# Kernel tuning notes

Hardware: AMD Instinct MI355X
Metric: run time of the kernel (lower is better)

Reference implementation:

```python
import jax, jax.numpy as jnp
import numpy as np

N_NODES = 20000
N_EDGES = 100000
STALK_DIM = 32
N_EDGE_ATTR = 32
N_FEAT = 32


def setup_inputs() -> dict:
    key = jax.random.key(0)
    k1, k2, k3, k4 = jax.random.split(key, 4)
    x = jax.random.normal(k1, (N_NODES, STALK_DIM, N_FEAT), dtype=jnp.float32)
    edge_index = jax.random.randint(k2, (2, N_EDGES), 0, N_NODES, dtype=jnp.int64)
    edge_attr = jax.random.normal(k3, (N_EDGES, N_EDGE_ATTR), dtype=jnp.float32)
    # basis restriction maps: (n_edge_attr, 2, d, d), scaled by 1/stalk_dim as in __init__
    restriction_maps = jax.random.normal(k4, (N_EDGE_ATTR, 2, STALK_DIM, STALK_DIM), dtype=jnp.float32) / STALK_DIM
    return {"x": x, "edge_index": edge_index, "edge_attr": edge_attr, "restriction_maps": restriction_maps}


def reference(x, edge_index, edge_attr, restriction_maps):
    n_nodes, d, _ = x.shape
    n_attr = restriction_maps.shape[0]
    # per-edge restriction maps via linear combination of basis maps
    # F: (E, 2, d, d)
    F = (edge_attr @ restriction_maps.reshape(n_attr, 2 * d * d)).reshape(-1, 2, d, d)
    F_left = F[:, 0]   # (E, d, d)
    F_right = F[:, 1]  # (E, d, d)
    # gather node features onto edges
    x_left = x[edge_index[0]]   # (E, d, f)
    x_right = x[edge_index[1]]  # (E, d, f)
    # coboundary: dx = F_left @ x_left - F_right @ x_right
    dx = jnp.einsum('eij,ejf->eif', F_left, x_left) - jnp.einsum('eij,ejf->eif', F_right, x_right)
    # boundary (delta^T dx): transpose-apply and scatter-add to nodes
    x_e_left = jnp.einsum('eji,ejf->eif', F_left, dx)    # F_left^T @ dx
    x_e_right = jnp.einsum('eji,ejf->eif', F_right, dx)  # F_right^T @ dx
    x_out = jax.ops.segment_sum(x_e_left, edge_index[0], num_segments=n_nodes)
    x_out = x_out - jax.ops.segment_sum(x_e_right, edge_index[1], num_segments=n_nodes)
    return x_out
```

## Files before the change

kernel.cpp:

```cpp
#include <hip/hip_runtime.h>
#include <hip/hip_bf16.h>

#define NN 20000
#define NE 100000
#define NINC (2 * NE)
#define NB (NINC / 16)
#define PGRID 512
#define SLOTS 16
#define FSTRIDE 2056

typedef __attribute__((ext_vector_type(8))) short bf16x8;
typedef __attribute__((ext_vector_type(4))) float f32x4;
typedef __attribute__((ext_vector_type(16))) float f32x16;
typedef __attribute__((ext_vector_type(2))) unsigned uint2v;
typedef __attribute__((ext_vector_type(4))) unsigned uint4v;

#define WS_RBFT 0u
#define WS_FLAG 131072u
#define WS_OFF  131328u
#define WS_CUR  (WS_OFF + 4u*(NN+1))
#define WS_CNT  (WS_CUR + 4u*NN)
#define WS_INC  (WS_CNT + 4u*NN)
#define WS_NODE (WS_INC + 4u*NINC)
#define WS_CSR_END ((size_t)WS_NODE + 4u*NINC)
#define WS_XT   ((WS_CSR_END + 4095u) & ~(size_t)4095u)
#define WS_XT_END (WS_XT + (size_t)NN * 2048u * 2u)
#define WS_PB   ((WS_XT_END + 4095u) & ~(size_t)4095u)
#define WS_PB_END (WS_PB + (size_t)NB * 2u * 2048u)

__device__ __forceinline__ unsigned short f2bf(float f) {
    unsigned u = __float_as_uint(f);
    u += 0x7fffu + ((u >> 16) & 1u);
    return (unsigned short)(u >> 16);
}

__device__ __forceinline__ unsigned pack2bf(float a, float b) {
    union { __hip_bfloat162 h; unsigned u; } q;
    q.h = __float22bfloat162_rn(make_float2(a, b));
    return q.u;
}

__device__ __forceinline__ float bf2f(unsigned s) {
    return __uint_as_float(s << 16);
}

__device__ __forceinline__ bf16x8 bneg8(bf16x8 v) {
    union { bf16x8 s; uint4v u; } a; a.s = v;
    a.u[0] ^= 0x80008000u; a.u[1] ^= 0x80008000u;
    a.u[2] ^= 0x80008000u; a.u[3] ^= 0x80008000u;
    return a.s;
}

__global__ void prep_rbf_kernel(const float* __restrict__ R, unsigned short* __restrict__ RbfT,
                                int* __restrict__ flag) {
    int idx = blockIdx.x * blockDim.x + threadIdx.x;
    if (idx == 0) *flag = 0;
    if (idx >= 2048 * 32) return;
    int pos = idx >> 5;
    int a = idx & 31;
    RbfT[idx] = f2bf(R[a * 2048 + pos]);
}

__global__ void detect_kernel(const unsigned* __restrict__ w, int* __restrict__ flag) {
    int k = blockIdx.x * blockDim.x + threadIdx.x;
    if (k < NE && w[2 * k + 1] != 0) atomicOr(flag, 1);
}

__device__ __forceinline__ void decode_edge(const void* eidx, int use64, int e, int& src, int& dst) {
    if (use64) {
        const long long* p = (const long long*)eidx;
        src = (int)p[e]; dst = (int)p[NE + e];
    } else {
        const int* p = (const int*)eidx;
        src = p[e]; dst = p[NE + e];
    }
}

__global__ void count_kernel(const void* __restrict__ eidx, const int* __restrict__ flag,
                             unsigned* __restrict__ cnt) {
    int e = blockIdx.x * blockDim.x + threadIdx.x;
    if (e >= NE) return;
    int src, dst;
    decode_edge(eidx, *flag == 0, e, src, dst);
    if ((unsigned)src < NN) atomicAdd(&cnt[src], 1u);
    if ((unsigned)dst < NN) atomicAdd(&cnt[dst], 1u);
}

__global__ __launch_bounds__(1024) void scan_kernel(const unsigned* __restrict__ cnt,
                                                    unsigned* __restrict__ off,
                                                    unsigned* __restrict__ cur) {
    __shared__ unsigned sd[1024];
    const int t = threadIdx.x;
    unsigned vals[20];
    unsigned s = 0;
#pragma unroll
    for (int j = 0; j < 20; ++j) {
        int idx = t * 20 + j;
        unsigned v = (idx < NN) ? cnt[idx] : 0u;
        vals[j] = s; s += v;
    }
    sd[t] = s;
    __syncthreads();
    for (int d = 1; d < 1024; d <<= 1) {
        unsigned v = (t >= d) ? sd[t - d] : 0u;
        __syncthreads();
        sd[t] += v;
        __syncthreads();
    }
    unsigned base = (t > 0) ? sd[t - 1] : 0u;
#pragma unroll
    for (int j = 0; j < 20; ++j) {
        int idx = t * 20 + j;
        if (idx < NN) { unsigned o = base + vals[j]; off[idx] = o; cur[idx] = o; }
    }
    if (t == 1023) off[NN] = sd[1023];
}

__global__ void scatter_kernel(const void* __restrict__ eidx, const int* __restrict__ flag,
                               unsigned* __restrict__ cur, unsigned* __restrict__ inc,
                               unsigned* __restrict__ nodeOf) {
    int e = blockIdx.x * blockDim.x + threadIdx.x;
    if (e >= NE) return;
    int src, dst;
    decode_edge(eidx, *flag == 0, e, src, dst);
    if ((unsigned)src < NN) { unsigned p = atomicAdd(&cur[src], 1u); inc[p] = (unsigned)e; nodeOf[p] = (unsigned)src; }
    if ((unsigned)dst < NN) { unsigned p = atomicAdd(&cur[dst], 1u); inc[p] = (unsigned)e | 0x80000000u; nodeOf[p] = (unsigned)dst; }
}

__global__ __launch_bounds__(256) void xpose_kernel(const float* __restrict__ x,
                                                    unsigned short* __restrict__ xT) {
    __shared__ float tile[4][32][33];
    const int t = threadIdx.x, sub = t >> 6, lane = t & 63;
    const int n = blockIdx.x * 4 + sub;
    const int row = lane >> 1, half = (lane & 1) * 16;
    const float* xp = x + (size_t)n * 1024 + row * 32 + half;
    float* tp = &tile[sub][row][half];
#pragma unroll
    for (int c = 0; c < 4; ++c)
        *(f32x4*)(tp + 4 * c) = *(const f32x4*)(xp + 4 * c);
    __syncthreads();
    const int f = lane >> 1, k0 = (lane & 1) * 16;
    unsigned w[8];
#pragma unroll
    for (int m = 0; m < 8; ++m) {
        unsigned lo = (unsigned)f2bf(tile[sub][k0 + 2 * m][f]);
        unsigned hi = (unsigned)f2bf(tile[sub][k0 + 2 * m + 1][f]);
        w[m] = lo | (hi << 16);
    }
    unsigned short* op = xT + (size_t)n * 2048 + f * 32 + k0;
    uint4v v0 = {w[0], w[1], w[2], w[3]};
    uint4v v1 = {w[4], w[5], w[6], w[7]};
    *(uint4v*)op = v0;
    *(uint4v*)(op + 8) = v1;
}

__global__ __launch_bounds__(256, 2) void sheaf_inc(
    const unsigned short* __restrict__ xTbuf,
    const void* __restrict__ eidx_raw,
    const float* __restrict__ ea,
    const unsigned short* __restrict__ RbfT,
    const int* __restrict__ flag,
    const unsigned* __restrict__ off,
    const unsigned* __restrict__ inc,
    const unsigned* __restrict__ nodeOf,
    float* __restrict__ out,
    unsigned short* __restrict__ pbuf)
{
    __shared__ __align__(16) unsigned short F_lds[SLOTS * FSTRIDE];
    __shared__ __align__(16) unsigned dx_lds32[4 * 512];
    __shared__ int slot_src[SLOTS], slot_dst[SLOTS], slot_side[SLOTS], slot_e[SLOTS], slot_n[SLOTS];

    const int tid  = threadIdx.x;
    const int lane = tid & 63;
    const int wv   = tid >> 6;
    const int use64 = (*flag == 0);

    const int r31 = lane & 31;
    const int hi  = lane >> 5;
    const int kb  = hi * 8;
    const int l15 = lane & 15;
    const int ab  = (lane >> 4) * 8;
    const int pg  = (lane >> 4) * 4;
    unsigned* dx2 = dx_lds32 + wv * 512;

    bf16x8 rbft[32];
#pragma unroll
    for (int t = 0; t < 32; ++t)
        rbft[t] = *(const bf16x8*)(RbfT + (size_t)(wv * 512 + t * 16 + l15) * 32 + ab);

    for (int b = blockIdx.x; b < NB; b += PGRID) {
        const int p0 = b * 16;
        __syncthreads();

        if (tid < SLOTS) {
            unsigned v = inc[p0 + tid];
            int e = (int)(v & 0x7fffffffu);
            int s, d; decode_edge(eidx_raw, use64, e, s, d);
            if ((unsigned)s >= NN) s = 0;
            if ((unsigned)d >= NN) d = 0;
            slot_e[tid] = e; slot_src[tid] = s; slot_dst[tid] = d;
            slot_side[tid] = (int)(v >> 31);
            slot_n[tid] = (int)nodeOf[p0 + tid];
        }
        __syncthreads();

        bf16x8 pre0[4], pre1[4], pre2[4], pre3[4];
#pragma unroll
        for (int s = 0; s < 4; ++s) {
            const int si = wv + 4 * s;
            const unsigned short* xls = xTbuf + (size_t)slot_src[si] * 2048 + r31 * 32 + kb;
            const unsigned short* xrs = xTbuf + (size_t)slot_dst[si] * 2048 + r31 * 32 + kb;
            pre0[s] = *(const bf16x8*)xls;
            pre1[s] = *(const bf16x8*)(xls + 16);
            pre2[s] = *(const bf16x8*)xrs;
            pre3[s] = *(const bf16x8*)(xrs + 16);
        }

        {
            const int e = slot_e[l15];
            bf16x8 bfrag;
            {
                const float* eap = ea + (size_t)e * 32 + ab;
                f32x4 a0 = *(const f32x4*)eap;
                f32x4 a1 = *(const f32x4*)(eap + 4);
#pragma unroll
                for (int j = 0; j < 4; ++j) { bfrag[j] = (short)f2bf(a0[j]); bfrag[4 + j] = (short)f2bf(a1[j]); }
            }
            unsigned short* fdst = F_lds + l15 * FSTRIDE;
#pragma unroll
            for (int t = 0; t < 32; ++t) {
                f32x4 c = {0.f, 0.f, 0.f, 0.f};
                c = __builtin_amdgcn_mfma_f32_16x16x32_bf16(rbft[t], bfrag, c, 0, 0, 0);
                const int posb = wv * 512 + t * 16 + pg;
                const int side = posb >> 10;
                const int ijb  = posb & 1023;
                const int i    = ijb >> 5;
                const int soff = ijb ^ ((i & 7) << 3);
                uint2v wp = {pack2bf(c[0], c[1]), pack2bf(c[2], c[3])};
                *(uint2v*)(fdst + side * 1024 + soff) = wp;
            }
        }
        __syncthreads();

#pragma unroll
        for (int s = 0; s < 4; ++s) {
            const int si = wv + 4 * s;
            const int side = slot_side[si];

            bf16x8 xlf0 = pre0[s];
            bf16x8 xlf1 = pre1[s];
            bf16x8 xrf0 = bneg8(pre2[s]);
            bf16x8 xrf1 = bneg8(pre3[s]);

            const unsigned short* Fl = F_lds + si * FSTRIDE;
            const unsigned short* Fr = Fl + 1024;
            const int rbase = r31 * 32;
            const int rsw   = (r31 & 7) << 3;
            bf16x8 fl0 = *(const bf16x8*)(Fl + ((rbase + kb) ^ rsw));
            bf16x8 fl1 = *(const bf16x8*)(Fl + ((rbase + 16 + kb) ^ rsw));
            bf16x8 fr0 = *(const bf16x8*)(Fr + ((rbase + kb) ^ rsw));
            bf16x8 fr1 = *(const bf16x8*)(Fr + ((rbase + 16 + kb) ^ rsw));

            f32x16 dacc;
#pragma unroll
            for (int r = 0; r < 16; ++r) dacc[r] = 0.f;
            dacc = __builtin_amdgcn_mfma_f32_32x32x16_bf16(fl0, xlf0, dacc, 0, 0, 0);
            dacc = __builtin_amdgcn_mfma_f32_32x32x16_bf16(fl1, xlf1, dacc, 0, 0, 0);
            dacc = __builtin_amdgcn_mfma_f32_32x32x16_bf16(fr0, xrf0, dacc, 0, 0, 0);
            dacc = __builtin_amdgcn_mfma_f32_32x32x16_bf16(fr1, xrf1, dacc, 0, 0, 0);

            const unsigned smask = side ? 0x80008000u : 0u;
#pragma unroll
            for (int m = 0; m < 8; ++m) {
                const int wi = (m & 1) + 4 * (m >> 1) + 2 * hi;
                dx2[wi * 32 + r31] = pack2bf(dacc[2 * m], dacc[2 * m + 1]) ^ smask;
            }
            unsigned wa[4], wb[4];
#pragma unroll
            for (int m = 0; m < 4; ++m) {
                wa[m] = dx2[(4 * hi + m) * 32 + r31];
                wb[m] = dx2[(8 + 4 * hi + m) * 32 + r31];
            }
            union { uint4v u; bf16x8 s; } pa, pb;
            pa.u = (uint4v){wa[0], wa[1], wa[2], wa[3]};
            pb.u = (uint4v){wb[0], wb[1], wb[2], wb[3]};
            const bf16x8 dxf0 = pa.s, dxf1 = pb.s;

            const unsigned short* Fs = side ? Fr : Fl;
            bf16x8 fT0, fT1;
#pragma unroll
            for (int j = 0; j < 8; ++j) {
                const int k0 = kb + j, k1 = 16 + kb + j;
                fT0[j] = (short)Fs[(k0 * 32 + r31) ^ ((k0 & 7) << 3)];
                fT1[j] = (short)Fs[(k1 * 32 + r31) ^ ((k1 & 7) << 3)];
            }
            f32x16 y;
#pragma unroll
            for (int r = 0; r < 16; ++r) y[r] = 0.f;
            y = __builtin_amdgcn_mfma_f32_32x32x16_bf16(fT0, dxf0, y, 0, 0, 0);
            y = __builtin_amdgcn_mfma_f32_32x32x16_bf16(fT1, dxf1, y, 0, 0, 0);

            float* ybuf = (float*)(F_lds + si * FSTRIDE);
#pragma unroll
            for (int r = 0; r < 16; ++r) {
                const int row = (r & 3) + 8 * (r >> 2) + 4 * hi;
                ybuf[row * 32 + r31] = y[r];
            }
        }
        __syncthreads();

        {
            const int e4 = tid * 4;
            int segA = 0;
            while (segA < SLOTS) {
                const int n = slot_n[segA];
                int segB = segA + 1;
                while (segB < SLOTS && slot_n[segB] == n) ++segB;
                f32x4 sum = {0.f, 0.f, 0.f, 0.f};
                for (int s2 = segA; s2 < segB; ++s2) {
                    const f32x4 v = *(const f32x4*)((const float*)(F_lds + s2 * FSTRIDE) + e4);
#pragma unroll
                    for (int j = 0; j < 4; ++j) sum[j] += v[j];
                }
                const unsigned on = off[n], on1 = off[n + 1];
                const bool complete = ((unsigned)(p0 + segA) == on) && ((unsigned)(p0 + segB) == on1);
                if (complete) {
                    *(f32x4*)(out + (size_t)n * 1024 + e4) = sum;
                } else {
                    const int idx = (segA == 0) ? 0 : 1;
                    unsigned short* pb = pbuf + ((size_t)b * 2 + idx) * 1024;
                    uint2v wp = {pack2bf(sum[0], sum[1]), pack2bf(sum[2], sum[3])};
                    *(uint2v*)(pb + e4) = wp;
                }
                segA = segB;
            }
        }
    }
}

__global__ __launch_bounds__(256) void combine_kernel(
    const unsigned* __restrict__ off, const unsigned* __restrict__ nodeOf,
    const unsigned short* __restrict__ pbuf, float* __restrict__ out)
{
    const int n = blockIdx.x;
    const int e4 = threadIdx.x * 4;
    const unsigned a = off[n], b = off[n + 1];
    if (a == b) {
        f32x4 z = {0.f, 0.f, 0.f, 0.f};
        *(f32x4*)(out + (size_t)n * 1024 + e4) = z;
        return;
    }
    const unsigned b0 = a >> 4, b1 = (b - 1) >> 4;
    if (b0 == b1) return;
    f32x4 sum = {0.f, 0.f, 0.f, 0.f};
    for (unsigned blk = b0; blk <= b1; ++blk) {
        const int idx = (nodeOf[blk * 16] == (unsigned)n) ? 0 : 1;
        const unsigned short* pb = pbuf + ((size_t)blk * 2 + idx) * 1024;
        uint2v w = *(const uint2v*)(pb + e4);
        sum[0] += bf2f(w[0] & 0xffffu); sum[1] += bf2f(w[0] >> 16);
        sum[2] += bf2f(w[1] & 0xffffu); sum[3] += bf2f(w[1] >> 16);
    }
    *(f32x4*)(out + (size_t)n * 1024 + e4) = sum;
}

template<bool XT>
__global__ __launch_bounds__(256, 2) void sheaf_node(
    const float* __restrict__ x,
    const unsigned short* __restrict__ xTbuf,
    const void* __restrict__ eidx_raw,
    const float* __restrict__ ea,
    const unsigned short* __restrict__ RbfT,
    const int* __restrict__ flag,
    const unsigned* __restrict__ off,
    const unsigned* __restrict__ inc,
    float* __restrict__ out)
{
    __shared__ __align__(16) unsigned short F_lds[SLOTS * FSTRIDE];
    __shared__ __align__(16) unsigned dx_lds32[4 * 512];
    __shared__ int slot_src[SLOTS], slot_dst[SLOTS], slot_side[SLOTS], slot_e[SLOTS];

    const int n    = blockIdx.x;
    const int tid  = threadIdx.x;
    const int lane = tid & 63;
    const int wv   = tid >> 6;
    const int use64 = (*flag == 0);

    const unsigned start = off[n];
    const int deg = (int)(off[n + 1] - start);

    const int r31 = lane & 31;
    const int hi  = lane >> 5;
    const int kb  = hi * 8;
    unsigned* dx2 = dx_lds32 + wv * 512;

    f32x16 acc;
#pragma unroll
    for (int r = 0; r < 16; ++r) acc[r] = 0.f;

    for (int base = 0; base < deg; base += SLOTS) {
        __syncthreads();
        if (tid < SLOTS) {
            int p = base + tid;
            if (p < deg) {
                unsigned v = inc[start + p];
                int e = (int)(v & 0x7fffffffu);
                int s, d; decode_edge(eidx_raw, use64, e, s, d);
                if ((unsigned)s >= NN) s = 0;
                if ((unsigned)d >= NN) d = 0;
                slot_e[tid] = e; slot_src[tid] = s; slot_dst[tid] = d;
                slot_side[tid] = (int)(v >> 31);
            } else slot_e[tid] = -1;
        }
        __syncthreads();

        bf16x8 pre0[4], pre1[4], pre2[4], pre3[4];
        if constexpr (XT) {
#pragma unroll
            for (int s = 0; s < 4; ++s) {
                const int si = wv + 4 * s;
                if (base + si < deg) {
                    const unsigned short* xls = xTbuf + (size_t)slot_src[si] * 2048 + r31 * 32 + kb;
                    const unsigned short* xrs = xTbuf + (size_t)slot_dst[si] * 2048 + r31 * 32 + kb;
                    pre0[s] = *(const bf16x8*)xls;
                    pre1[s] = *(const bf16x8*)(xls + 16);
                    pre2[s] = *(const bf16x8*)xrs;
                    pre3[s] = *(const bf16x8*)(xrs + 16);
                }
            }
        }

        {
            const int slot = lane & 15;
            const int ab   = (lane >> 4) * 8;
            const int e    = slot_e[slot];
            bf16x8 bfrag = {0, 0, 0, 0, 0, 0, 0, 0};
            if (e >= 0) {
                const float* eap = ea + (size_t)e * 32 + ab;
                f32x4 a0 = *(const f32x4*)eap;
                f32x4 a1 = *(const f32x4*)(eap + 4);
#pragma unroll
                for (int j = 0; j < 4; ++j) { bfrag[j] = (short)f2bf(a0[j]); bfrag[4 + j] = (short)f2bf(a1[j]); }
            }
            unsigned short* fdst = F_lds + slot * FSTRIDE;
            const int pg = (lane >> 4) * 4;
#pragma unroll 8
            for (int t = 0; t < 32; ++t) {
                const int pos_base = wv * 512 + t * 16;
                bf16x8 afrag = *(const bf16x8*)(RbfT + (size_t)(pos_base + (lane & 15)) * 32 + ab);
                f32x4 c = {0.f, 0.f, 0.f, 0.f};
                c = __builtin_amdgcn_mfma_f32_16x16x32_bf16(afrag, bfrag, c, 0, 0, 0);
                const int posb = pos_base + pg;
                const int side = posb >> 10;
                const int ijb  = posb & 1023;
                const int i    = ijb >> 5;
                const int soff = ijb ^ ((i & 7) << 3);
                uint2v wp = {pack2bf(c[0], c[1]), pack2bf(c[2], c[3])};
                *(uint2v*)(fdst + side * 1024 + soff) = wp;
            }
        }
        __syncthreads();

#pragma unroll
        for (int s = 0; s < 4; ++s) {
            const int si = wv + 4 * s;
            if (base + si >= deg) break;
            const int src  = slot_src[si];
            const int dst  = slot_dst[si];
            const int side = slot_side[si];

            bf16x8 xlf0, xlf1, xrf0, xrf1;
            if constexpr (XT) {
                xlf0 = pre0[s];
                xlf1 = pre1[s];
                xrf0 = bneg8(pre2[s]);
                xrf1 = bneg8(pre3[s]);
            } else {
                const float* xl = x + (size_t)src * 1024 + r31;
                const float* xr = x + (size_t)dst * 1024 + r31;
#pragma unroll
                for (int j = 0; j < 8; ++j) {
                    xlf0[j] = (short)f2bf(xl[(kb + j) * 32]);
                    xlf1[j] = (short)f2bf(xl[(16 + kb + j) * 32]);
                    xrf0[j] = (short)f2bf(-xr[(kb + j) * 32]);
                    xrf1[j] = (short)f2bf(-xr[(16 + kb + j) * 32]);
                }
            }

            const unsigned short* Fl = F_lds + si * FSTRIDE;
            const unsigned short* Fr = Fl + 1024;
            const int rbase = r31 * 32;
            const int rsw   = (r31 & 7) << 3;
            bf16x8 fl0 = *(const bf16x8*)(Fl + ((rbase + kb) ^ rsw));
            bf16x8 fl1 = *(const bf16x8*)(Fl + ((rbase + 16 + kb) ^ rsw));
            bf16x8 fr0 = *(const bf16x8*)(Fr + ((rbase + kb) ^ rsw));
            bf16x8 fr1 = *(const bf16x8*)(Fr + ((rbase + 16 + kb) ^ rsw));

            f32x16 dacc;
#pragma unroll
            for (int r = 0; r < 16; ++r) dacc[r] = 0.f;
            dacc = __builtin_amdgcn_mfma_f32_32x32x16_bf16(fl0, xlf0, dacc, 0, 0, 0);
            dacc = __builtin_amdgcn_mfma_f32_32x32x16_bf16(fl1, xlf1, dacc, 0, 0, 0);
            dacc = __builtin_amdgcn_mfma_f32_32x32x16_bf16(fr0, xrf0, dacc, 0, 0, 0);
            dacc = __builtin_amdgcn_mfma_f32_32x32x16_bf16(fr1, xrf1, dacc, 0, 0, 0);

            const unsigned smask = side ? 0x80008000u : 0u;
#pragma unroll
            for (int m = 0; m < 8; ++m) {
                const int wi = (m & 1) + 4 * (m >> 1) + 2 * hi;
                dx2[wi * 32 + r31] = pack2bf(dacc[2 * m], dacc[2 * m + 1]) ^ smask;
            }
            unsigned wa[4], wb[4];
#pragma unroll
            for (int m = 0; m < 4; ++m) {
                wa[m] = dx2[(4 * hi + m) * 32 + r31];
                wb[m] = dx2[(8 + 4 * hi + m) * 32 + r31];
            }
            union { uint4v u; bf16x8 s; } pa, pb;
            pa.u = (uint4v){wa[0], wa[1], wa[2], wa[3]};
            pb.u = (uint4v){wb[0], wb[1], wb[2], wb[3]};
            const bf16x8 dxf0 = pa.s, dxf1 = pb.s;

            const unsigned short* Fs = side ? Fr : Fl;
            bf16x8 fT0, fT1;
#pragma unroll
            for (int j = 0; j < 8; ++j) {
                const int k0 = kb + j, k1 = 16 + kb + j;
                fT0[j] = (short)Fs[(k0 * 32 + r31) ^ ((k0 & 7) << 3)];
                fT1[j] = (short)Fs[(k1 * 32 + r31) ^ ((k1 & 7) << 3)];
            }
            acc = __builtin_amdgcn_mfma_f32_32x32x16_bf16(fT0, dxf0, acc, 0, 0, 0);
            acc = __builtin_amdgcn_mfma_f32_32x32x16_bf16(fT1, dxf1, acc, 0, 0, 0);
        }
    }

    __syncthreads();
    float* red = (float*)F_lds;
#pragma unroll
    for (int r = 0; r < 16; ++r) {
        const int row = (r & 3) + 8 * (r >> 2) + 4 * hi;
        red[wv * 1024 + row * 32 + r31] = acc[r];
    }
    __syncthreads();
    {
        const int p4 = tid * 4;
        f32x4 s0 = *(const f32x4*)(red + p4);
        f32x4 s1 = *(const f32x4*)(red + 1024 + p4);
        f32x4 s2 = *(const f32x4*)(red + 2048 + p4);
        f32x4 s3 = *(const f32x4*)(red + 3072 + p4);
        f32x4 o;
#pragma unroll
        for (int j = 0; j < 4; ++j) o[j] = (s0[j] + s1[j]) + (s2[j] + s3[j]);
        *(f32x4*)(out + (size_t)n * 1024 + p4) = o;
    }
}

__global__ __launch_bounds__(512, 4) void sheaf_atomic(
    const float* __restrict__ x,
    const void* __restrict__ eidx_raw,
    const float* __restrict__ ea,
    const unsigned short* __restrict__ RbfT,
    const int* __restrict__ flag,
    float* __restrict__ out)
{
    __shared__ __align__(16) unsigned short F_lds[16 * 2048];
    __shared__ __align__(16) unsigned short dx_lds[8 * 1024];

    const int tid  = threadIdx.x;
    const int lane = tid & 63;
    const int wv   = tid >> 6;
    const int e0   = blockIdx.x * 16;
    const int use64 = (*flag == 0);

    {
        const int arow = lane & 15;
        const int ab   = (lane >> 4) * 8;
        const float* eap = ea + (size_t)(e0 + arow) * 32 + ab;
        f32x4 a0 = *(const f32x4*)eap;
        f32x4 a1 = *(const f32x4*)(eap + 4);
        bf16x8 afrag;
#pragma unroll
        for (int j = 0; j < 4; ++j) { afrag[j] = (short)f2bf(a0[j]); afrag[4 + j] = (short)f2bf(a1[j]); }
        const int pcol  = lane & 15;
        const int ebase = (lane >> 4) * 4;
#pragma unroll
        for (int t = 0; t < 16; ++t) {
            const int pos = wv * 256 + t * 16 + pcol;
            bf16x8 bfrag = *(const bf16x8*)(RbfT + pos * 32 + ab);
            f32x4 c = {0.f, 0.f, 0.f, 0.f};
            c = __builtin_amdgcn_mfma_f32_16x16x32_bf16(afrag, bfrag, c, 0, 0, 0);
            const int side = pos >> 10;
            const int ij   = pos & 1023;
            const int i    = ij >> 5;
            const int soff = side * 1024 + (ij ^ ((i & 7) << 3));
#pragma unroll
            for (int r = 0; r < 4; ++r)
                F_lds[(ebase + r) * 2048 + soff] = f2bf(c[r]);
        }
    }
    __syncthreads();

    const int r31 = lane & 31;
    const int hi  = lane >> 5;
    const int kb  = hi * 8;
    unsigned short* dxb = dx_lds + wv * 1024;

#pragma unroll 1
    for (int sub = 0; sub < 2; ++sub) {
        const int el = wv * 2 + sub;
        const int e  = e0 + el;
        int src, dst;
        decode_edge(eidx_raw, use64, e, src, dst);
        if ((unsigned)src >= NN || (unsigned)dst >= NN) continue;

        const float* xl = x + (size_t)src * 1024 + r31;
        const float* xr = x + (size_t)dst * 1024 + r31;
        bf16x8 xlf0, xlf1, xrf0, xrf1;
#pragma unroll
        for (int j = 0; j < 8; ++j) {
            xlf0[j] = (short)f2bf(xl[(kb + j) * 32]);
            xlf1[j] = (short)f2bf(xl[(16 + kb + j) * 32]);
            xrf0[j] = (short)f2bf(-xr[(kb + j) * 32]);
            xrf1[j] = (short)f2bf(-xr[(16 + kb + j) * 32]);
        }
        const unsigned short* Fl = F_lds + el * 2048;
        const unsigned short* Fr = Fl + 1024;
        const int rbase = r31 * 32;
        const int rsw   = (r31 & 7) << 3;
        bf16x8 fl0 = *(const bf16x8*)(Fl + ((rbase + kb) ^ rsw));
        bf16x8 fl1 = *(const bf16x8*)(Fl + ((rbase + 16 + kb) ^ rsw));
        bf16x8 fr0 = *(const bf16x8*)(Fr + ((rbase + kb) ^ rsw));
        bf16x8 fr1 = *(const bf16x8*)(Fr + ((rbase + 16 + kb) ^ rsw));

        f32x16 dacc;
#pragma unroll
        for (int r = 0; r < 16; ++r) dacc[r] = 0.f;
        dacc = __builtin_amdgcn_mfma_f32_32x32x16_bf16(fl0, xlf0, dacc, 0, 0, 0);
        dacc = __builtin_amdgcn_mfma_f32_32x32x16_bf16(fl1, xlf1, dacc, 0, 0, 0);
        dacc = __builtin_amdgcn_mfma_f32_32x32x16_bf16(fr0, xrf0, dacc, 0, 0, 0);
        dacc = __builtin_amdgcn_mfma_f32_32x32x16_bf16(fr1, xrf1, dacc, 0, 0, 0);

#pragma unroll
        for (int r = 0; r < 16; ++r) {
            const int row = (r & 3) + 8 * (r >> 2) + 4 * hi;
            dxb[row * 32 + r31] = f2bf(dacc[r]);
        }
        bf16x8 dxf0, dxf1;
#pragma unroll
        for (int j = 0; j < 8; ++j) {
            dxf0[j] = (short)dxb[(kb + j) * 32 + r31];
            dxf1[j] = (short)dxb[(16 + kb + j) * 32 + r31];
        }

        bf16x8 flT0, flT1;
#pragma unroll
        for (int j = 0; j < 8; ++j) {
            const int k0 = kb + j, k1 = 16 + kb + j;
            flT0[j] = (short)Fl[(k0 * 32 + r31) ^ ((k0 & 7) << 3)];
            flT1[j] = (short)Fl[(k1 * 32 + r31) ^ ((k1 & 7) << 3)];
        }
        f32x16 yl;
#pragma unroll
        for (int r = 0; r < 16; ++r) yl[r] = 0.f;
        yl = __builtin_amdgcn_mfma_f32_32x32x16_bf16(flT0, dxf0, yl, 0, 0, 0);
        yl = __builtin_amdgcn_mfma_f32_32x32x16_bf16(flT1, dxf1, yl, 0, 0, 0);
        float* outs = out + (size_t)src * 1024 + r31;
#pragma unroll
        for (int r = 0; r < 16; ++r) {
            const int row = (r & 3) + 8 * (r >> 2) + 4 * hi;
            atomicAdd(outs + row * 32, yl[r]);
        }

        bf16x8 frT0, frT1;
#pragma unroll
        for (int j = 0; j < 8; ++j) {
            const int k0 = kb + j, k1 = 16 + kb + j;
            frT0[j] = (short)Fr[(k0 * 32 + r31) ^ ((k0 & 7) << 3)];
            frT1[j] = (short)Fr[(k1 * 32 + r31) ^ ((k1 & 7) << 3)];
        }
        f32x16 yr;
#pragma unroll
        for (int r = 0; r < 16; ++r) yr[r] = 0.f;
        yr = __builtin_amdgcn_mfma_f32_32x32x16_bf16(frT0, dxf0, yr, 0, 0, 0);
        yr = __builtin_amdgcn_mfma_f32_32x32x16_bf16(frT1, dxf1, yr, 0, 0, 0);
        float* outd = out + (size_t)dst * 1024 + r31;
#pragma unroll
        for (int r = 0; r < 16; ++r) {
            const int row = (r & 3) + 8 * (r >> 2) + 4 * hi;
            atomicAdd(outd + row * 32, -yr[r]);
        }
    }
}

extern "C" void kernel_launch(void* const* d_in, const int* in_sizes, int n_in,
                              void* d_out, int out_size, void* d_ws, size_t ws_size,
                              hipStream_t stream) {
    const float* x  = (const float*)d_in[0];
    const void* eidx = d_in[1];
    const float* ea = (const float*)d_in[2];
    const float* R  = (const float*)d_in[3];
    float* out = (float*)d_out;
    char* ws = (char*)d_ws;

    unsigned short* RbfT = (unsigned short*)(ws + WS_RBFT);
    int* flag = (int*)(ws + WS_FLAG);

    prep_rbf_kernel<<<256, 256, 0, stream>>>(R, RbfT, flag);
    detect_kernel<<<(NE + 255) / 256, 256, 0, stream>>>((const unsigned*)eidx, flag);

    if (ws_size >= WS_CSR_END) {
        unsigned* off = (unsigned*)(ws + WS_OFF);
        unsigned* cur = (unsigned*)(ws + WS_CUR);
        unsigned* cnt = (unsigned*)(ws + WS_CNT);
        unsigned* inc = (unsigned*)(ws + WS_INC);
        unsigned* nodeOf = (unsigned*)(ws + WS_NODE);

        hipMemsetAsync(cnt, 0, 4u * NN, stream);
        count_kernel<<<(NE + 255) / 256, 256, 0, stream>>>(eidx, flag, cnt);
        scan_kernel<<<1, 1024, 0, stream>>>(cnt, off, cur);
        scatter_kernel<<<(NE + 255) / 256, 256, 0, stream>>>(eidx, flag, cur, inc, nodeOf);

        if (ws_size >= WS_PB_END) {
            unsigned short* xT = (unsigned short*)(ws + WS_XT);
            unsigned short* pbuf = (unsigned short*)(ws + WS_PB);
            xpose_kernel<<<NN / 4, 256, 0, stream>>>(x, xT);
            sheaf_inc<<<PGRID, 256, 0, stream>>>(xT, eidx, ea, RbfT, flag, off, inc, nodeOf, out, pbuf);
            combine_kernel<<<NN, 256, 0, stream>>>(off, nodeOf, pbuf, out);
        } else if (ws_size >= WS_XT_END) {
            unsigned short* xT = (unsigned short*)(ws + WS_XT);
            xpose_kernel<<<NN / 4, 256, 0, stream>>>(x, xT);
            sheaf_node<true><<<NN, 256, 0, stream>>>(x, xT, eidx, ea, RbfT, flag, off, inc, out);
        } else {
            sheaf_node<false><<<NN, 256, 0, stream>>>(x, nullptr, eidx, ea, RbfT, flag, off, inc, out);
        }
    } else {
        hipMemsetAsync(d_out, 0, (size_t)out_size * sizeof(float), stream);
        sheaf_atomic<<<NE / 16, 512, 0, stream>>>(x, eidx, ea, RbfT, flag, out);
    }
}
```

Before: 346.7 us.

## Double-buffer per-block slot metadata and prefetch next block's edge attributes

Slot metadata (edge ids, endpoints, side, node, CSR offsets) for the next 16-incidence block is now decoded into a second shared buffer while the current block computes. Edge-attribute rows for the next block are prefetched into registers, and the node offsets are cached in shared memory instead of being reloaded in the scatter phase. This removes one barrier and a dependent global-load chain at the start of each iteration. In exchange it uses slightly more shared memory and registers.

Result: slower. 359.6 us (+3.7%).

```diff
diff --git a/kernel.cpp b/kernel.cpp
--- a/kernel.cpp
+++ b/kernel.cpp
@@ -168,7 +168,8 @@
 {
     __shared__ __align__(16) unsigned short F_lds[SLOTS * FSTRIDE];
     __shared__ __align__(16) unsigned dx_lds32[4 * 512];
-    __shared__ int slot_src[SLOTS], slot_dst[SLOTS], slot_side[SLOTS], slot_e[SLOTS], slot_n[SLOTS];
+    __shared__ int sl_src[2][16], sl_dst[2][16], sl_side[2][16], sl_e[2][16], sl_n[2][16];
+    __shared__ unsigned sl_o0[2][16], sl_o1[2][16];
 
     const int tid  = threadIdx.x;
     const int lane = tid & 63;
@@ -188,44 +189,67 @@
     for (int t = 0; t < 32; ++t)
         rbft[t] = *(const bf16x8*)(RbfT + (size_t)(wv * 512 + t * 16 + l15) * 32 + ab);
 
-    for (int b = blockIdx.x; b < NB; b += PGRID) {
+    int b = blockIdx.x;
+    if (tid < SLOTS) {
+        const int q = 0;
+        unsigned v = inc[b * 16 + tid];
+        int e = (int)(v & 0x7fffffffu);
+        int s, d; decode_edge(eidx_raw, use64, e, s, d);
+        if ((unsigned)s >= NN) s = 0;
+        if ((unsigned)d >= NN) d = 0;
+        sl_e[q][tid] = e; sl_src[q][tid] = s; sl_dst[q][tid] = d;
+        sl_side[q][tid] = (int)(v >> 31);
+        int n = (int)nodeOf[b * 16 + tid];
+        sl_n[q][tid] = n;
+        sl_o0[q][tid] = off[n];
+        sl_o1[q][tid] = off[n + 1];
+    }
+    __syncthreads();
+
+    f32x4 eaA, eaB;
+    {
+        const float* eap = ea + (size_t)sl_e[0][l15] * 32 + ab;
+        eaA = *(const f32x4*)eap;
+        eaB = *(const f32x4*)(eap + 4);
+    }
+
+    int par = 0;
+    while (true) {
         const int p0 = b * 16;
-        __syncthreads();
-
-        if (tid < SLOTS) {
-            unsigned v = inc[p0 + tid];
+        const int bn = b + PGRID;
+        const bool has_next = bn < NB;
+        const int nxt = par ^ 1;
+
+        bf16x8 pre0[4], pre1[4], pre2[4], pre3[4];
+#pragma unroll
+        for (int s = 0; s < 4; ++s) {
+            const int si = wv + 4 * s;
+            const unsigned short* xls = xTbuf + (size_t)sl_src[par][si] * 2048 + r31 * 32 + kb;
+            const unsigned short* xrs = xTbuf + (size_t)sl_dst[par][si] * 2048 + r31 * 32 + kb;
+            pre0[s] = *(const bf16x8*)xls;
+            pre1[s] = *(const bf16x8*)(xls + 16);
+            pre2[s] = *(const bf16x8*)xrs;
+            pre3[s] = *(const bf16x8*)(xrs + 16);
+        }
+
+        if (has_next && tid < SLOTS) {
+            unsigned v = inc[bn * 16 + tid];
             int e = (int)(v & 0x7fffffffu);
             int s, d; decode_edge(eidx_raw, use64, e, s, d);
             if ((unsigned)s >= NN) s = 0;
             if ((unsigned)d >= NN) d = 0;
-            slot_e[tid] = e; slot_src[tid] = s; slot_dst[tid] = d;
-            slot_side[tid] = (int)(v >> 31);
-            slot_n[tid] = (int)nodeOf[p0 + tid];
-        }
-        __syncthreads();
-
-        bf16x8 pre0[4], pre1[4], pre2[4], pre3[4];
-#pragma unroll
-        for (int s = 0; s < 4; ++s) {
-            const int si = wv + 4 * s;
-            const unsigned short* xls = xTbuf + (size_t)slot_src[si] * 2048 + r31 * 32 + kb;
-            const unsigned short* xrs = xTbuf + (size_t)slot_dst[si] * 2048 + r31 * 32 + kb;
-            pre0[s] = *(const bf16x8*)xls;
-            pre1[s] = *(const bf16x8*)(xls + 16);
-            pre2[s] = *(const bf16x8*)xrs;
-            pre3[s] = *(const bf16x8*)(xrs + 16);
+            sl_e[nxt][tid] = e; sl_src[nxt][tid] = s; sl_dst[nxt][tid] = d;
+            sl_side[nxt][tid] = (int)(v >> 31);
+            int n = (int)nodeOf[bn * 16 + tid];
+            sl_n[nxt][tid] = n;
+            sl_o0[nxt][tid] = off[n];
+            sl_o1[nxt][tid] = off[n + 1];
         }
 
         {
-            const int e = slot_e[l15];
             bf16x8 bfrag;
-            {
-                const float* eap = ea + (size_t)e * 32 + ab;
-                f32x4 a0 = *(const f32x4*)eap;
-                f32x4 a1 = *(const f32x4*)(eap + 4);
-#pragma unroll
-                for (int j = 0; j < 4; ++j) { bfrag[j] = (short)f2bf(a0[j]); bfrag[4 + j] = (short)f2bf(a1[j]); }
-            }
+#pragma unroll
+            for (int j = 0; j < 4; ++j) { bfrag[j] = (short)f2bf(eaA[j]); bfrag[4 + j] = (short)f2bf(eaB[j]); }
             unsigned short* fdst = F_lds + l15 * FSTRIDE;
 #pragma unroll
             for (int t = 0; t < 32; ++t) {
@@ -242,10 +266,16 @@
         }
         __syncthreads();
 
+        if (has_next) {
+            const float* eap = ea + (size_t)sl_e[nxt][l15] * 32 + ab;
+            eaA = *(const f32x4*)eap;
+            eaB = *(const f32x4*)(eap + 4);
+        }
+
 #pragma unroll
         for (int s = 0; s < 4; ++s) {
             const int si = wv + 4 * s;
-            const int side = slot_side[si];
+            const int side = sl_side[par][si];
 
             bf16x8 xlf0 = pre0[s];
             bf16x8 xlf1 = pre1[s];
@@ -313,16 +343,16 @@
             const int e4 = tid * 4;
             int segA = 0;
             while (segA < SLOTS) {
-                const int n = slot_n[segA];
+                const int n = sl_n[par][segA];
                 int segB = segA + 1;
-                while (segB < SLOTS && slot_n[segB] == n) ++segB;
+                while (segB < SLOTS && sl_n[par][segB] == n) ++segB;
                 f32x4 sum = {0.f, 0.f, 0.f, 0.f};
                 for (int s2 = segA; s2 < segB; ++s2) {
                     const f32x4 v = *(const f32x4*)((const float*)(F_lds + s2 * FSTRIDE) + e4);
 #pragma unroll
                     for (int j = 0; j < 4; ++j) sum[j] += v[j];
                 }
-                const unsigned on = off[n], on1 = off[n + 1];
+                const unsigned on = sl_o0[par][segA], on1 = sl_o1[par][segA];
                 const bool complete = ((unsigned)(p0 + segA) == on) && ((unsigned)(p0 + segB) == on1);
                 if (complete) {
                     *(f32x4*)(out + (size_t)n * 1024 + e4) = sum;
@@ -335,6 +365,11 @@
                 segA = segB;
             }
         }
+
+        if (!has_next) break;
+        __syncthreads();
+        b = bn;
+        par = nxt;
     }
 }
 
```
